# Kernel tuning notes

Hardware: AMD Instinct MI355X
Metric: run time of the kernel (lower is better)

## Reference

```python
import jax, jax.numpy as jnp
import numpy as np

N = 50000
E = 800000
F_IN = 128
HID = 32
NEG_SLOPE = 0.2  # PyG GATConv default


def _gat_layer(x, src, dst, W, a_src, a_dst, b, heads, out_c, concat, n_nodes):
    # Linear transform per head: [N, heads, out_c]
    h = (x @ W).reshape(n_nodes, heads, out_c)
    # Per-node attention logits per head
    al_src = jnp.einsum('nhc,hc->nh', h, a_src)  # source contribution
    al_dst = jnp.einsum('nhc,hc->nh', h, a_dst)  # destination contribution
    # Edge logits (message j=src -> i=dst), leaky relu
    e = jax.nn.leaky_relu(al_src[src] + al_dst[dst], NEG_SLOPE)  # [E', heads]
    # Segment softmax over incoming edges of each destination node
    m = jax.ops.segment_max(e, dst, num_segments=n_nodes)
    ex = jnp.exp(e - m[dst])
    denom = jax.ops.segment_sum(ex, dst, num_segments=n_nodes)
    alpha = ex / denom[dst]  # [E', heads]; self-loops guarantee denom > 0
    # Weighted scatter-aggregate of source features
    msg = h[src] * alpha[:, :, None]  # [E', heads, out_c]
    out = jax.ops.segment_sum(msg, dst, num_segments=n_nodes)  # [N, heads, out_c]
    out = out.reshape(n_nodes, heads * out_c) if concat else out.mean(axis=1)
    return out + b


def setup_inputs() -> dict:
    key = jax.random.key(0)
    ks = jax.random.split(key, 10)
    x = jax.random.normal(ks[0], (N, F_IN), dtype=jnp.float32)
    edge_index = jax.random.randint(ks[1], (2, E), 0, N, dtype=jnp.int64)
    s = 0.1
    return {
        'x': x,
        'edge_index': edge_index,
        'W1': jax.random.normal(ks[2], (F_IN, 4 * HID), dtype=jnp.float32) * s,
        'a_src1': jax.random.normal(ks[3], (4, HID), dtype=jnp.float32) * s,
        'a_dst1': jax.random.normal(ks[4], (4, HID), dtype=jnp.float32) * s,
        'b1': jnp.zeros((4 * HID,), jnp.float32),
        'W2': jax.random.normal(ks[5], (4 * HID, 2 * HID), dtype=jnp.float32) * s,
        'a_src2': jax.random.normal(ks[6], (2, HID), dtype=jnp.float32) * s,
        'a_dst2': jax.random.normal(ks[7], (2, HID), dtype=jnp.float32) * s,
        'b2': jnp.zeros((2 * HID,), jnp.float32),
        'W3': jax.random.normal(ks[8], (2 * HID, 1), dtype=jnp.float32) * s,
        'a_src3': jax.random.normal(ks[9], (1, 1), dtype=jnp.float32) * s,
        'a_dst3': jax.random.normal(jax.random.fold_in(key, 99), (1, 1), dtype=jnp.float32) * s,
        'b3': jnp.zeros((1,), jnp.float32),
    }


def reference(x, edge_index, W1, a_src1, a_dst1, b1, W2, a_src2, a_dst2, b2, W3, a_src3, a_dst3, b3):
    n = x.shape[0]
    # add_self_loops=True (PyG default)
    loop = jnp.arange(n, dtype=edge_index.dtype)
    src = jnp.concatenate([edge_index[0], loop])
    dst = jnp.concatenate([edge_index[1], loop])
    h = _gat_layer(x, src, dst, W1, a_src1, a_dst1, b1, 4, HID, True, n)
    h = jax.nn.elu(h)  # dropout is identity in eval mode
    h = _gat_layer(h, src, dst, W2, a_src2, a_dst2, b2, 2, HID, True, n)
    h = jax.nn.elu(h)
    out = _gat_layer(h, src, dst, W3, a_src3, a_dst3, b3, 1, 1, False, n)
    return out  # [N, 1]
```

## Files before the change

### kernel.cpp

```cpp
#include <hip/hip_runtime.h>
#include <hip/hip_fp16.h>
#include <math.h>

#define F_IN 128
constexpr int SB = 256;

__global__ void zero_int(int* p, int n) {
    int i = blockIdx.x * 256 + threadIdx.x;
    if (i < n) p[i] = 0;
}

__global__ void count_deg4(const int* __restrict__ dst, int* __restrict__ deg, int E) {
    int t = blockIdx.x * 256 + threadIdx.x;
    int base = t * 4;
    if (base + 3 < E) {
        int4 d = *(const int4*)(dst + base);
        atomicAdd(&deg[d.x], 1);
        atomicAdd(&deg[d.y], 1);
        atomicAdd(&deg[d.z], 1);
        atomicAdd(&deg[d.w], 1);
    } else {
        for (int k = 0; k < 4; ++k) {
            int e = base + k;
            if (e < E) atomicAdd(&deg[dst[e]], 1);
        }
    }
}

__global__ void scan1(const int* __restrict__ in, int* __restrict__ out,
                      int* __restrict__ bsums, int n, int selfN) {
    __shared__ int sm[SB];
    int i = blockIdx.x * SB + threadIdx.x;
    int v = (i < n) ? (in[i] + (i < selfN ? 1 : 0)) : 0;
    sm[threadIdx.x] = v;
    __syncthreads();
    for (int d = 1; d < SB; d <<= 1) {
        int t = (threadIdx.x >= d) ? sm[threadIdx.x - d] : 0;
        __syncthreads();
        sm[threadIdx.x] += t;
        __syncthreads();
    }
    if (i < n) out[i] = sm[threadIdx.x] - v;
    if (threadIdx.x == SB - 1) bsums[blockIdx.x] = sm[SB - 1];
}

__global__ void scan2(int* __restrict__ bsums, int nb) {
    __shared__ int sm[SB];
    int v = (threadIdx.x < nb) ? bsums[threadIdx.x] : 0;
    sm[threadIdx.x] = v;
    __syncthreads();
    for (int d = 1; d < SB; d <<= 1) {
        int t = (threadIdx.x >= d) ? sm[threadIdx.x - d] : 0;
        __syncthreads();
        sm[threadIdx.x] += t;
        __syncthreads();
    }
    if (threadIdx.x < nb) bsums[threadIdx.x] = sm[threadIdx.x] - v;
}

__global__ void scan3(int* __restrict__ off, int* __restrict__ cursor,
                      const int* __restrict__ bsums, int n, int ncur) {
    int i = blockIdx.x * SB + threadIdx.x;
    if (i < n) {
        int v = off[i] + bsums[blockIdx.x];
        off[i] = v;
        if (i < ncur) cursor[i] = v;
    }
}

template <int BN, int TN, int HEADS>
__device__ __forceinline__ void gemm_dev(
    const float* __restrict__ A, const float* __restrict__ B,
    const float* __restrict__ asrc, const float* __restrict__ adst,
    __half* __restrict__ C, float* __restrict__ als, float* __restrict__ ald,
    int M, int bid) {
    constexpr int BM = 128, BK = 16, TM = 4, K = 128, OC = 32;
    __shared__ float As[BK][BM + 4];
    __shared__ float Bs[BK][BN];
    const int tx = threadIdx.x, ty = threadIdx.y;
    const int tid = ty * 16 + tx;
    const int row0 = bid * BM;
    const int i0 = ty * TM;
    const int j0a = tx * 4;
    const int j0b = 64 + tx * 4;

    float acc[TM][TN];
#pragma unroll
    for (int m = 0; m < TM; ++m)
#pragma unroll
        for (int n = 0; n < TN; ++n) acc[m][n] = 0.f;

    const int ar = tid >> 2;
    const int ak = (tid & 3) * 4;
    int arow = row0 + ar;
    if (arow >= M) arow = M - 1;
    const float* Aptr = A + (size_t)arow * K + ak;
    const int bk = (BN == 128) ? (tid >> 5) : (tid >> 4);
    const int bc = (BN == 128) ? ((tid & 31) * 4) : ((tid & 15) * 4);
    const bool bact = (BN == 128) || (tid < 256);

    for (int kc = 0; kc < K; kc += BK) {
        float4 av = *(const float4*)(Aptr + kc);
        float4 bv;
        if (bact) bv = *(const float4*)(B + (size_t)(kc + bk) * BN + bc);
        __syncthreads();
        As[ak + 0][ar] = av.x;
        As[ak + 1][ar] = av.y;
        As[ak + 2][ar] = av.z;
        As[ak + 3][ar] = av.w;
        if (bact) *(float4*)&Bs[bk][bc] = bv;
        __syncthreads();
#pragma unroll
        for (int kk = 0; kk < BK; ++kk) {
            float4 a4 = *(const float4*)&As[kk][i0];
            float arr[TM] = {a4.x, a4.y, a4.z, a4.w};
            float br[TN];
            float4 b0 = *(const float4*)&Bs[kk][j0a];
            br[0] = b0.x; br[1] = b0.y; br[2] = b0.z; br[3] = b0.w;
            if constexpr (TN == 8) {
                float4 b1 = *(const float4*)&Bs[kk][j0b];
                br[4] = b1.x; br[5] = b1.y; br[6] = b1.z; br[7] = b1.w;
            }
#pragma unroll
            for (int m = 0; m < TM; ++m)
#pragma unroll
                for (int n = 0; n < TN; ++n) acc[m][n] += arr[m] * br[n];
        }
    }

#pragma unroll
    for (int m = 0; m < TM; ++m) {
        int row = row0 + i0 + m;
        bool ok = row < M;
        if constexpr (TN == 8) {
            if (ok) {
                alignas(8) __half2 pa[2], pb[2];
#pragma unroll
                for (int n2 = 0; n2 < 2; ++n2) {
                    pa[n2] = __floats2half2_rn(acc[m][2 * n2], acc[m][2 * n2 + 1]);
                    pb[n2] = __floats2half2_rn(acc[m][4 + 2 * n2], acc[m][5 + 2 * n2]);
                }
                *(uint2*)&C[(size_t)row * BN + j0a] = *(uint2*)pa;
                *(uint2*)&C[(size_t)row * BN + j0b] = *(uint2*)pb;
            }
            float psA = 0.f, pdA = 0.f, psB = 0.f, pdB = 0.f;
#pragma unroll
            for (int n = 0; n < 4; ++n) {
                psA += acc[m][n] * asrc[j0a + n];
                pdA += acc[m][n] * adst[j0a + n];
                psB += acc[m][n + 4] * asrc[j0b + n];
                pdB += acc[m][n + 4] * adst[j0b + n];
            }
#pragma unroll
            for (int msk = 1; msk < 8; msk <<= 1) {
                psA += __shfl_xor(psA, msk, 64);
                pdA += __shfl_xor(pdA, msk, 64);
                psB += __shfl_xor(psB, msk, 64);
                pdB += __shfl_xor(pdB, msk, 64);
            }
            if (ok && (tx & 7) == 0) {
                int hA = tx >> 3;
                als[row * HEADS + hA] = psA;
                ald[row * HEADS + hA] = pdA;
                als[row * HEADS + 2 + hA] = psB;
                ald[row * HEADS + 2 + hA] = pdB;
            }
        } else {
            if (ok) {
                alignas(8) __half2 ph[2];
#pragma unroll
                for (int n2 = 0; n2 < 2; ++n2)
                    ph[n2] = __floats2half2_rn(acc[m][2 * n2], acc[m][2 * n2 + 1]);
                *(uint2*)&C[(size_t)row * BN + j0a] = *(uint2*)ph;
            }
            float ps = 0.f, pd = 0.f;
#pragma unroll
            for (int n = 0; n < TN; ++n) {
                ps += acc[m][n] * asrc[j0a + n];
                pd += acc[m][n] * adst[j0a + n];
            }
#pragma unroll
            for (int msk = 1; msk < 8; msk <<= 1) {
                ps += __shfl_xor(ps, msk, 64);
                pd += __shfl_xor(pd, msk, 64);
            }
            if (ok && (tx & 7) == 0) {
                int h0 = tx >> 3;
                als[row * HEADS + h0] = ps;
                ald[row * HEADS + h0] = pd;
            }
        }
    }
}

__global__ __launch_bounds__(512) void gemm1_scatter(
    const float* __restrict__ A, const float* __restrict__ B,
    const float* __restrict__ asrc, const float* __restrict__ adst,
    __half* __restrict__ C, float* __restrict__ als, float* __restrict__ ald,
    int M, int gblk,
    const int* __restrict__ src, const int* __restrict__ dst,
    int* __restrict__ cursor, int* __restrict__ csr, int E, int N) {
    if ((int)blockIdx.x < gblk) {
        gemm_dev<128, 8, 4>(A, B, asrc, adst, C, als, ald, M, blockIdx.x);
        return;
    }
    int tid = threadIdx.y * 16 + threadIdx.x;
    int g = blockIdx.x & 7;
    int c = (blockIdx.x - gblk) >> 3;
    int t = c * 512 + tid;
    int E4 = (E + 3) >> 2;
    int nspan = (N + 7) >> 3;
    int r0 = g * nspan;
    int r1 = r0 + nspan; if (r1 > N) r1 = N;
    if (t < E4) {
        int base = t * 4;
        if (base + 3 < E) {
            int4 s4 = *(const int4*)(src + base);
            int4 d4 = *(const int4*)(dst + base);
            if (d4.x >= r0 && d4.x < r1) { int p = atomicAdd(&cursor[d4.x], 1); csr[p] = s4.x; }
            if (d4.y >= r0 && d4.y < r1) { int p = atomicAdd(&cursor[d4.y], 1); csr[p] = s4.y; }
            if (d4.z >= r0 && d4.z < r1) { int p = atomicAdd(&cursor[d4.z], 1); csr[p] = s4.z; }
            if (d4.w >= r0 && d4.w < r1) { int p = atomicAdd(&cursor[d4.w], 1); csr[p] = s4.w; }
        } else {
            for (int k = 0; k < 4; ++k) {
                int e = base + k;
                if (e < E) {
                    int d = dst[e];
                    if (d >= r0 && d < r1) {
                        int p = atomicAdd(&cursor[d], 1);
                        csr[p] = src[e];
                    }
                }
            }
        }
    } else {
        int i = t - E4;
        if (i >= r0 && i < r1) {
            int p = atomicAdd(&cursor[i], 1);
            csr[p] = i;
        }
    }
}

template <int BN, int TN, int HEADS>
__global__ __launch_bounds__(512) void gemm_fused(
    const float* __restrict__ A, const float* __restrict__ B,
    const float* __restrict__ asrc, const float* __restrict__ adst,
    __half* __restrict__ C, float* __restrict__ als, float* __restrict__ ald,
    int M) {
    gemm_dev<BN, TN, HEADS>(A, B, asrc, adst, C, als, ald, M, blockIdx.x);
}

template <int HEADS>
__global__ void edge_ex_node(const float* __restrict__ als, const float* __restrict__ ald,
                             const int* __restrict__ csr, const int* __restrict__ off,
                             float* __restrict__ ex_t, int n, int ET) {
    int g = blockIdx.x * blockDim.x + threadIdx.x;
    int node = g >> 4;
    int lane = g & 15;
    if (node >= n) return;
    float ad[HEADS];
    if constexpr (HEADS == 4) {
        float4 a = ((const float4*)ald)[node];
        ad[0] = a.x; ad[1] = a.y; ad[2] = a.z; ad[3] = a.w;
    } else if constexpr (HEADS == 2) {
        float2 a = ((const float2*)ald)[node];
        ad[0] = a.x; ad[1] = a.y;
    } else {
        ad[0] = ald[node];
    }
    int e1 = off[node + 1];
    for (int e = off[node] + lane; e < e1; e += 16) {
        int s = csr[e];
        float av[HEADS];
        if constexpr (HEADS == 4) {
            float4 a = ((const float4*)als)[s];
            av[0] = a.x; av[1] = a.y; av[2] = a.z; av[3] = a.w;
        } else if constexpr (HEADS == 2) {
            float2 a = ((const float2*)als)[s];
            av[0] = a.x; av[1] = a.y;
        } else {
            av[0] = als[s];
        }
#pragma unroll
        for (int hd = 0; hd < HEADS; ++hd) {
            float lg = av[hd] + ad[hd];
            lg = lg > 0.f ? lg : 0.2f * lg;
            ex_t[(size_t)hd * ET + e] = __expf(lg);
        }
    }
}

__global__ void gat_agg_l1(const __half* __restrict__ h, const float* __restrict__ ex_t,
                           const float* __restrict__ bias,
                           const int* __restrict__ off, const int* __restrict__ csr,
                           float* __restrict__ out, int n, int ET) {
    constexpr int P = 8;
    int wid = (blockIdx.x * blockDim.x + threadIdx.x) >> 6;
    int lane = threadIdx.x & 63;
    if (wid >= n) return;
    const int hd = lane >> 4;
    const __half2* h2 = (const __half2*)h + lane;
    const float* exp_ = ex_t + (size_t)hd * ET;
    int e0 = off[wid], e1 = off[wid + 1];
    float Sx = 0.f, Sy = 0.f, D = 0.f;

    float ex[P];
    __half2 hv[P];
#pragma unroll
    for (int p = 0; p < P; ++p) {
        int ee = e0 + p;
        int ie = (ee < e1) ? ee : e1 - 1;
        int s = csr[ie];
        float exv = exp_[ie];
        ex[p] = (ee < e1) ? exv : 0.f;
        hv[p] = h2[(size_t)s * 64];
    }
    int e = e0;
    for (; e + P < e1; e += P) {
        float nex[P];
        __half2 nhv[P];
#pragma unroll
        for (int p = 0; p < P; ++p) {
            int ee = e + P + p;
            int ie = (ee < e1) ? ee : e1 - 1;
            int s = csr[ie];
            float exv = exp_[ie];
            nex[p] = (ee < e1) ? exv : 0.f;
            nhv[p] = h2[(size_t)s * 64];
        }
#pragma unroll
        for (int p = 0; p < P; ++p) {
            D += ex[p];
            Sx = fmaf(ex[p], __low2float(hv[p]), Sx);
            Sy = fmaf(ex[p], __high2float(hv[p]), Sy);
            ex[p] = nex[p];
            hv[p] = nhv[p];
        }
    }
#pragma unroll
    for (int p = 0; p < P; ++p) {
        D += ex[p];
        Sx = fmaf(ex[p], __low2float(hv[p]), Sx);
        Sy = fmaf(ex[p], __high2float(hv[p]), Sy);
    }

    float inv = 1.f / D;
    float2 bv = ((const float2*)bias)[lane];
    float vx = Sx * inv + bv.x, vy = Sy * inv + bv.y;
    vx = vx > 0.f ? vx : (__expf(vx) - 1.f);
    vy = vy > 0.f ? vy : (__expf(vy) - 1.f);
    float2 o; o.x = vx; o.y = vy;
    ((float2*)out)[(size_t)wid * 64 + lane] = o;
}

__global__ void gat_agg_l2(const __half* __restrict__ h, const float* __restrict__ ex_t,
                           const float* __restrict__ bias,
                           const int* __restrict__ off, const int* __restrict__ csr,
                           const float* __restrict__ W3, const float* __restrict__ as3,
                           const float* __restrict__ ad3, float* __restrict__ h3,
                           float* __restrict__ als3, float* __restrict__ ald3,
                           int n, int ET) {
    constexpr int P = 8;
    int wid = (blockIdx.x * blockDim.x + threadIdx.x) >> 6;
    int lane = threadIdx.x & 63;
    if (wid >= n) return;
    const int hd = lane >> 5;
    const __half* hp = h + lane;
    const float* exp_ = ex_t + (size_t)hd * ET;
    int e0 = off[wid], e1 = off[wid + 1];
    float S = 0.f, D = 0.f;

    float ex[P];
    __half hv[P];
#pragma unroll
    for (int p = 0; p < P; ++p) {
        int ee = e0 + p;
        int ie = (ee < e1) ? ee : e1 - 1;
        int s = csr[ie];
        float exv = exp_[ie];
        ex[p] = (ee < e1) ? exv : 0.f;
        hv[p] = hp[(size_t)s * 64];
    }
    int e = e0;
    for (; e + P < e1; e += P) {
        float nex[P];
        __half nhv[P];
#pragma unroll
        for (int p = 0; p < P; ++p) {
            int ee = e + P + p;
            int ie = (ee < e1) ? ee : e1 - 1;
            int s = csr[ie];
            float exv = exp_[ie];
            nex[p] = (ee < e1) ? exv : 0.f;
            nhv[p] = hp[(size_t)s * 64];
        }
#pragma unroll
        for (int p = 0; p < P; ++p) {
            D += ex[p];
            S = fmaf(ex[p], __half2float(hv[p]), S);
            ex[p] = nex[p];
            hv[p] = nhv[p];
        }
    }
#pragma unroll
    for (int p = 0; p < P; ++p) {
        D += ex[p];
        S = fmaf(ex[p], __half2float(hv[p]), S);
    }

    float v = S / D + bias[lane];
    v = v > 0.f ? v : (__expf(v) - 1.f);
    float r = v * W3[lane];
#pragma unroll
    for (int msk = 1; msk < 64; msk <<= 1) r += __shfl_xor(r, msk, 64);
    if (lane == 0) {
        h3[wid] = r;
        als3[wid] = r * as3[0];
        ald3[wid] = r * ad3[0];
    }
}

__global__ void gat_agg1(const float* __restrict__ h, const float* __restrict__ ex_t,
                         const float* __restrict__ bias,
                         const int* __restrict__ off, const int* __restrict__ csr,
                         float* __restrict__ out, int n) {
    int i = blockIdx.x * blockDim.x + threadIdx.x;
    if (i >= n) return;
    int e0 = off[i], e1 = off[i + 1];
    float S = 0.f, D = 0.f;
    float ex[2], hv[2];
#pragma unroll
    for (int p = 0; p < 2; ++p) {
        int ee = e0 + p;
        int ie = (ee < e1) ? ee : e1 - 1;
        int s = csr[ie];
        float exv = ex_t[ie];
        ex[p] = (ee < e1) ? exv : 0.f;
        hv[p] = h[s];
    }
    int e = e0;
    for (; e + 2 < e1; e += 2) {
#pragma unroll
        for (int p = 0; p < 2; ++p) {
            int ee = e + 2 + p;
            int ie = (ee < e1) ? ee : e1 - 1;
            int s = csr[ie];
            float exv = ex_t[ie];
            float nex = (ee < e1) ? exv : 0.f;
            float nhv = h[s];
            D += ex[p];
            S = fmaf(ex[p], hv[p], S);
            ex[p] = nex;
            hv[p] = nhv;
        }
    }
#pragma unroll
    for (int p = 0; p < 2; ++p) {
        D += ex[p];
        S = fmaf(ex[p], hv[p], S);
    }
    out[i] = S / D + bias[0];
}

extern "C" void kernel_launch(void* const* d_in, const int* in_sizes, int n_in,
                              void* d_out, int out_size, void* d_ws, size_t ws_size,
                              hipStream_t stream) {
    const float* x   = (const float*)d_in[0];
    const int*   ei  = (const int*)d_in[1];
    const float* W1  = (const float*)d_in[2];
    const float* as1 = (const float*)d_in[3];
    const float* ad1 = (const float*)d_in[4];
    const float* b1  = (const float*)d_in[5];
    const float* W2  = (const float*)d_in[6];
    const float* as2 = (const float*)d_in[7];
    const float* ad2 = (const float*)d_in[8];
    const float* b2  = (const float*)d_in[9];
    const float* W3  = (const float*)d_in[10];
    const float* as3 = (const float*)d_in[11];
    const float* ad3 = (const float*)d_in[12];
    const float* b3  = (const float*)d_in[13];
    float* out = (float*)d_out;

    const int N = in_sizes[0] / F_IN;
    const int E = in_sizes[1] / 2;
    const int ET = E + N;

    char* w = (char*)d_ws;
    size_t o = 0;
    auto alloc = [&](size_t bytes) -> void* {
        void* p = w + o;
        o += (bytes + 255) & ~(size_t)255;
        return p;
    };
    __half* hbuf = (__half*)alloc((size_t)N * 128 * 2);
    float* a1   = (float*)alloc((size_t)N * 128 * 4);
    float* h3   = (float*)alloc((size_t)N * 4);
    float* als  = (float*)alloc((size_t)N * 4 * 4);
    float* ald  = (float*)alloc((size_t)N * 4 * 4);
    float* als3 = (float*)alloc((size_t)N * 4);
    float* ald3 = (float*)alloc((size_t)N * 4);
    int* deg    = (int*)alloc((size_t)(N + 1) * 4);
    int* off    = (int*)alloc((size_t)(N + 1) * 4);
    int* cursor = (int*)alloc((size_t)N * 4);
    int* bsums  = (int*)alloc(1024);
    int* csr    = (int*)alloc((size_t)ET * 4);
    float* exb  = (float*)alloc((size_t)4 * ET * 4);

    __half* h2 = hbuf;

    const int* esrc = ei;
    const int* edst = ei + E;

    zero_int<<<(N + 1 + 255) / 256, 256, 0, stream>>>(deg, N + 1);
    count_deg4<<<((E + 3) / 4 + 255) / 256, 256, 0, stream>>>(edst, deg, E);
    int n1 = N + 1;
    int nb = (n1 + SB - 1) / SB;
    scan1<<<nb, SB, 0, stream>>>(deg, off, bsums, n1, N);
    scan2<<<1, SB, 0, stream>>>(bsums, nb);
    scan3<<<nb, SB, 0, stream>>>(off, cursor, bsums, n1, N);

    const int gblk = (N + 127) / 128;

    {
        int E4 = (E + 3) >> 2;
        int spg = (E4 + N + 511) / 512;
        int sblk = 8 * spg;
        gemm1_scatter<<<gblk + sblk, dim3(16, 32), 0, stream>>>(
            x, W1, as1, ad1, hbuf, als, ald, N, gblk,
            esrc, edst, cursor, csr, E, N);
    }

    const int exblk = (N * 16 + 255) / 256;

    edge_ex_node<4><<<exblk, 256, 0, stream>>>(als, ald, csr, off, exb, N, ET);
    gat_agg_l1<<<(N * 64 + 255) / 256, 256, 0, stream>>>(
        hbuf, exb, b1, off, csr, a1, N, ET);

    gemm_fused<64, 4, 2><<<gblk, dim3(16, 32), 0, stream>>>(
        a1, W2, as2, ad2, h2, als, ald, N);
    edge_ex_node<2><<<exblk, 256, 0, stream>>>(als, ald, csr, off, exb, N, ET);
    gat_agg_l2<<<(N * 64 + 255) / 256, 256, 0, stream>>>(
        h2, exb, b2, off, csr, W3, as3, ad3, h3, als3, ald3, N, ET);

    edge_ex_node<1><<<exblk, 256, 0, stream>>>(als3, ald3, csr, off, exb, N, ET);
    gat_agg1<<<(N + 255) / 256, 256, 0, stream>>>(h3, exb, b3, off, csr, out, N);
}
```

Baseline: 219.5 us.

## Fuse edge exp computation into aggregation kernels and store layer-1 output in fp16

Removes the three separate edge_ex_node kernels and the per-edge exp buffer; each aggregation kernel now gathers the source logit and computes leaky-relu plus exp inline. The layer-1 activations are stored as fp16 and the layer-2 GEMM reads half inputs. Layer 3 packs h and its source logit into one float2 so a single gather serves both. Zeroing uses hipMemsetAsync instead of a kernel. This saves launches and per-edge global traffic, at the cost of recomputing exp per lane and lower precision for the intermediate activations.

```diff
diff --git a/kernel.cpp b/kernel.cpp
--- a/kernel.cpp
+++ b/kernel.cpp
@@ -4,11 +4,6 @@
 
 #define F_IN 128
 constexpr int SB = 256;
-
-__global__ void zero_int(int* p, int n) {
-    int i = blockIdx.x * 256 + threadIdx.x;
-    if (i < n) p[i] = 0;
-}
 
 __global__ void count_deg4(const int* __restrict__ dst, int* __restrict__ deg, int E) {
     int t = blockIdx.x * 256 + threadIdx.x;
@@ -68,13 +63,13 @@
     }
 }
 
-template <int BN, int TN, int HEADS>
+template <int BN, int TN, int HEADS, typename AT>
 __device__ __forceinline__ void gemm_dev(
-    const float* __restrict__ A, const float* __restrict__ B,
+    const AT* __restrict__ A, const float* __restrict__ B,
     const float* __restrict__ asrc, const float* __restrict__ adst,
     __half* __restrict__ C, float* __restrict__ als, float* __restrict__ ald,
     int M, int bid) {
-    constexpr int BM = 128, BK = 16, TM = 4, K = 128, OC = 32;
+    constexpr int BM = 128, BK = 16, TM = 4, K = 128;
     __shared__ float As[BK][BM + 4];
     __shared__ float Bs[BK][BN];
     const int tx = threadIdx.x, ty = threadIdx.y;
@@ -94,20 +89,31 @@
     const int ak = (tid & 3) * 4;
     int arow = row0 + ar;
     if (arow >= M) arow = M - 1;
-    const float* Aptr = A + (size_t)arow * K + ak;
+    const AT* Aptr = A + (size_t)arow * K + ak;
     const int bk = (BN == 128) ? (tid >> 5) : (tid >> 4);
     const int bc = (BN == 128) ? ((tid & 31) * 4) : ((tid & 15) * 4);
     const bool bact = (BN == 128) || (tid < 256);
 
     for (int kc = 0; kc < K; kc += BK) {
-        float4 av = *(const float4*)(Aptr + kc);
+        float a0, a1v, a2v, a3v;
+        if constexpr (sizeof(AT) == 4) {
+            float4 av = *(const float4*)(Aptr + kc);
+            a0 = av.x; a1v = av.y; a2v = av.z; a3v = av.w;
+        } else {
+            uint2 raw = *(const uint2*)(Aptr + kc);
+            __half2 h01 = *(__half2*)&raw.x;
+            __half2 h23 = *(__half2*)&raw.y;
+            float2 f01 = __half22float2(h01);
+            float2 f23 = __half22float2(h23);
+            a0 = f01.x; a1v = f01.y; a2v = f23.x; a3v = f23.y;
+        }
         float4 bv;
         if (bact) bv = *(const float4*)(B + (size_t)(kc + bk) * BN + bc);
         __syncthreads();
-        As[ak + 0][ar] = av.x;
-        As[ak + 1][ar] = av.y;
-        As[ak + 2][ar] = av.z;
-        As[ak + 3][ar] = av.w;
+        As[ak + 0][ar] = a0;
+        As[ak + 1][ar] = a1v;
+        As[ak + 2][ar] = a2v;
+        As[ak + 3][ar] = a3v;
         if (bact) *(float4*)&Bs[bk][bc] = bv;
         __syncthreads();
 #pragma unroll
@@ -201,7 +207,7 @@
     const int* __restrict__ src, const int* __restrict__ dst,
     int* __restrict__ cursor, int* __restrict__ csr, int E, int N) {
     if ((int)blockIdx.x < gblk) {
-        gemm_dev<128, 8, 4>(A, B, asrc, adst, C, als, ald, M, blockIdx.x);
+        gemm_dev<128, 8, 4, float>(A, B, asrc, adst, C, als, ald, M, blockIdx.x);
         return;
     }
     int tid = threadIdx.y * 16 + threadIdx.x;
@@ -243,106 +249,73 @@
 }
 
 template <int BN, int TN, int HEADS>
-__global__ __launch_bounds__(512) void gemm_fused(
-    const float* __restrict__ A, const float* __restrict__ B,
+__global__ __launch_bounds__(512) void gemm_fused_h(
+    const __half* __restrict__ A, const float* __restrict__ B,
     const float* __restrict__ asrc, const float* __restrict__ adst,
     __half* __restrict__ C, float* __restrict__ als, float* __restrict__ ald,
     int M) {
-    gemm_dev<BN, TN, HEADS>(A, B, asrc, adst, C, als, ald, M, blockIdx.x);
-}
-
-template <int HEADS>
-__global__ void edge_ex_node(const float* __restrict__ als, const float* __restrict__ ald,
-                             const int* __restrict__ csr, const int* __restrict__ off,
-                             float* __restrict__ ex_t, int n, int ET) {
-    int g = blockIdx.x * blockDim.x + threadIdx.x;
-    int node = g >> 4;
-    int lane = g & 15;
-    if (node >= n) return;
-    float ad[HEADS];
-    if constexpr (HEADS == 4) {
-        float4 a = ((const float4*)ald)[node];
-        ad[0] = a.x; ad[1] = a.y; ad[2] = a.z; ad[3] = a.w;
-    } else if constexpr (HEADS == 2) {
-        float2 a = ((const float2*)ald)[node];
-        ad[0] = a.x; ad[1] = a.y;
-    } else {
-        ad[0] = ald[node];
-    }
-    int e1 = off[node + 1];
-    for (int e = off[node] + lane; e < e1; e += 16) {
-        int s = csr[e];
-        float av[HEADS];
-        if constexpr (HEADS == 4) {
-            float4 a = ((const float4*)als)[s];
-            av[0] = a.x; av[1] = a.y; av[2] = a.z; av[3] = a.w;
-        } else if constexpr (HEADS == 2) {
-            float2 a = ((const float2*)als)[s];
-            av[0] = a.x; av[1] = a.y;
-        } else {
-            av[0] = als[s];
-        }
-#pragma unroll
-        for (int hd = 0; hd < HEADS; ++hd) {
-            float lg = av[hd] + ad[hd];
-            lg = lg > 0.f ? lg : 0.2f * lg;
-            ex_t[(size_t)hd * ET + e] = __expf(lg);
-        }
-    }
-}
-
-__global__ void gat_agg_l1(const __half* __restrict__ h, const float* __restrict__ ex_t,
+    gemm_dev<BN, TN, HEADS, __half>(A, B, asrc, adst, C, als, ald, M, blockIdx.x);
+}
+
+__global__ void gat_agg_l1(const __half* __restrict__ h,
+                           const float* __restrict__ als, const float* __restrict__ ald,
                            const float* __restrict__ bias,
                            const int* __restrict__ off, const int* __restrict__ csr,
-                           float* __restrict__ out, int n, int ET) {
+                           __half* __restrict__ out, int n) {
     constexpr int P = 8;
     int wid = (blockIdx.x * blockDim.x + threadIdx.x) >> 6;
     int lane = threadIdx.x & 63;
     if (wid >= n) return;
     const int hd = lane >> 4;
     const __half2* h2 = (const __half2*)h + lane;
-    const float* exp_ = ex_t + (size_t)hd * ET;
+    float ad = ald[wid * 4 + hd];
     int e0 = off[wid], e1 = off[wid + 1];
     float Sx = 0.f, Sy = 0.f, D = 0.f;
 
-    float ex[P];
+    float al[P];
     __half2 hv[P];
 #pragma unroll
     for (int p = 0; p < P; ++p) {
         int ee = e0 + p;
         int ie = (ee < e1) ? ee : e1 - 1;
         int s = csr[ie];
-        float exv = exp_[ie];
-        ex[p] = (ee < e1) ? exv : 0.f;
+        float av = als[s * 4 + hd];
+        al[p] = (ee < e1) ? av : -1e30f;
         hv[p] = h2[(size_t)s * 64];
     }
     int e = e0;
     for (; e + P < e1; e += P) {
-        float nex[P];
+        float nal[P];
         __half2 nhv[P];
 #pragma unroll
         for (int p = 0; p < P; ++p) {
             int ee = e + P + p;
             int ie = (ee < e1) ? ee : e1 - 1;
             int s = csr[ie];
-            float exv = exp_[ie];
-            nex[p] = (ee < e1) ? exv : 0.f;
+            float av = als[s * 4 + hd];
+            nal[p] = (ee < e1) ? av : -1e30f;
             nhv[p] = h2[(size_t)s * 64];
         }
 #pragma unroll
         for (int p = 0; p < P; ++p) {
-            D += ex[p];
-            Sx = fmaf(ex[p], __low2float(hv[p]), Sx);
-            Sy = fmaf(ex[p], __high2float(hv[p]), Sy);
-            ex[p] = nex[p];
+            float lg = al[p] + ad;
+            lg = lg > 0.f ? lg : 0.2f * lg;
+            float exv = __expf(lg);
+            D += exv;
+            Sx = fmaf(exv, __low2float(hv[p]), Sx);
+            Sy = fmaf(exv, __high2float(hv[p]), Sy);
+            al[p] = nal[p];
             hv[p] = nhv[p];
         }
     }
 #pragma unroll
     for (int p = 0; p < P; ++p) {
-        D += ex[p];
-        Sx = fmaf(ex[p], __low2float(hv[p]), Sx);
-        Sy = fmaf(ex[p], __high2float(hv[p]), Sy);
+        float lg = al[p] + ad;
+        lg = lg > 0.f ? lg : 0.2f * lg;
+        float exv = __expf(lg);
+        D += exv;
+        Sx = fmaf(exv, __low2float(hv[p]), Sx);
+        Sy = fmaf(exv, __high2float(hv[p]), Sy);
     }
 
     float inv = 1.f / D;
@@ -350,63 +323,68 @@
     float vx = Sx * inv + bv.x, vy = Sy * inv + bv.y;
     vx = vx > 0.f ? vx : (__expf(vx) - 1.f);
     vy = vy > 0.f ? vy : (__expf(vy) - 1.f);
-    float2 o; o.x = vx; o.y = vy;
-    ((float2*)out)[(size_t)wid * 64 + lane] = o;
-}
-
-__global__ void gat_agg_l2(const __half* __restrict__ h, const float* __restrict__ ex_t,
+    ((__half2*)out)[(size_t)wid * 64 + lane] = __floats2half2_rn(vx, vy);
+}
+
+__global__ void gat_agg_l2(const __half* __restrict__ h,
+                           const float* __restrict__ als, const float* __restrict__ ald,
                            const float* __restrict__ bias,
                            const int* __restrict__ off, const int* __restrict__ csr,
                            const float* __restrict__ W3, const float* __restrict__ as3,
-                           const float* __restrict__ ad3, float* __restrict__ h3,
-                           float* __restrict__ als3, float* __restrict__ ald3,
-                           int n, int ET) {
+                           const float* __restrict__ ad3, float2* __restrict__ hs,
+                           float* __restrict__ ald3, int n) {
     constexpr int P = 8;
     int wid = (blockIdx.x * blockDim.x + threadIdx.x) >> 6;
     int lane = threadIdx.x & 63;
     if (wid >= n) return;
     const int hd = lane >> 5;
     const __half* hp = h + lane;
-    const float* exp_ = ex_t + (size_t)hd * ET;
+    float ad = ald[wid * 2 + hd];
     int e0 = off[wid], e1 = off[wid + 1];
     float S = 0.f, D = 0.f;
 
-    float ex[P];
+    float al[P];
     __half hv[P];
 #pragma unroll
     for (int p = 0; p < P; ++p) {
         int ee = e0 + p;
         int ie = (ee < e1) ? ee : e1 - 1;
         int s = csr[ie];
-        float exv = exp_[ie];
-        ex[p] = (ee < e1) ? exv : 0.f;
+        float av = als[s * 2 + hd];
+        al[p] = (ee < e1) ? av : -1e30f;
         hv[p] = hp[(size_t)s * 64];
     }
     int e = e0;
     for (; e + P < e1; e += P) {
-        float nex[P];
+        float nal[P];
         __half nhv[P];
 #pragma unroll
         for (int p = 0; p < P; ++p) {
             int ee = e + P + p;
             int ie = (ee < e1) ? ee : e1 - 1;
             int s = csr[ie];
-            float exv = exp_[ie];
-            nex[p] = (ee < e1) ? exv : 0.f;
+            float av = als[s * 2 + hd];
+            nal[p] = (ee < e1) ? av : -1e30f;
             nhv[p] = hp[(size_t)s * 64];
         }
 #pragma unroll
         for (int p = 0; p < P; ++p) {
-            D += ex[p];
-            S = fmaf(ex[p], __half2float(hv[p]), S);
-            ex[p] = nex[p];
+            float lg = al[p] + ad;
+            lg = lg > 0.f ? lg : 0.2f * lg;
+            float exv = __expf(lg);
+            D += exv;
+            S = fmaf(exv, __half2float(hv[p]), S);
+            al[p] = nal[p];
             hv[p] = nhv[p];
         }
     }
 #pragma unroll
     for (int p = 0; p < P; ++p) {
-        D += ex[p];
-        S = fmaf(ex[p], __half2float(hv[p]), S);
+        float lg = al[p] + ad;
+        lg = lg > 0.f ? lg : 0.2f * lg;
+        float exv = __expf(lg);
+        D += exv;
+        S = fmaf(exv, __half2float(hv[p]), S);
     }
 
     float v = S / D + bias[lane];
@@ -415,29 +393,29 @@
 #pragma unroll
     for (int msk = 1; msk < 64; msk <<= 1) r += __shfl_xor(r, msk, 64);
     if (lane == 0) {
-        h3[wid] = r;
-        als3[wid] = r * as3[0];
+        hs[wid] = make_float2(r, r * as3[0]);
         ald3[wid] = r * ad3[0];
     }
 }
 
-__global__ void gat_agg1(const float* __restrict__ h, const float* __restrict__ ex_t,
+__global__ void gat_agg1(const float2* __restrict__ hs, const float* __restrict__ ald3,
                          const float* __restrict__ bias,
                          const int* __restrict__ off, const int* __restrict__ csr,
                          float* __restrict__ out, int n) {
     int i = blockIdx.x * blockDim.x + threadIdx.x;
     if (i >= n) return;
+    float ad = ald3[i];
     int e0 = off[i], e1 = off[i + 1];
     float S = 0.f, D = 0.f;
-    float ex[2], hv[2];
+    float2 g[2];
+    float valid[2];
 #pragma unroll
     for (int p = 0; p < 2; ++p) {
         int ee = e0 + p;
         int ie = (ee < e1) ? ee : e1 - 1;
         int s = csr[ie];
-        float exv = ex_t[ie];
-        ex[p] = (ee < e1) ? exv : 0.f;
-        hv[p] = h[s];
+        g[p] = hs[s];
+        valid[p] = (ee < e1) ? 0.f : -1e30f;
     }
     int e = e0;
     for (; e + 2 < e1; e += 2) {
@@ -446,19 +424,24 @@
             int ee = e + 2 + p;
             int ie = (ee < e1) ? ee : e1 - 1;
             int s = csr[ie];
-            float exv = ex_t[ie];
-            float nex = (ee < e1) ? exv : 0.f;
-            float nhv = h[s];
-            D += ex[p];
-            S = fmaf(ex[p], hv[p], S);
-            ex[p] = nex;
-            hv[p] = nhv;
+            float2 ng = hs[s];
+            float nvalid = (ee < e1) ? 0.f : -1e30f;
+            float lg = g[p].y + ad + valid[p];
+            lg = lg > 0.f ? lg : 0.2f * lg;
+            float exv = __expf(lg);
+            D += exv;
+            S = fmaf(exv, g[p].x, S);
+            g[p] = ng;
+            valid[p] = nvalid;
         }
     }
 #pragma unroll
     for (int p = 0; p < 2; ++p) {
-        D += ex[p];
-        S = fmaf(ex[p], hv[p], S);
+        float lg = g[p].y + ad + valid[p];
+        lg = lg > 0.f ? lg : 0.2f * lg;
+        float exv = __expf(lg);
+        D += exv;
+        S = fmaf(exv, g[p].x, S);
     }
     out[i] = S / D + bias[0];
 }
@@ -494,25 +477,23 @@
         return p;
     };
     __half* hbuf = (__half*)alloc((size_t)N * 128 * 2);
-    float* a1   = (float*)alloc((size_t)N * 128 * 4);
-    float* h3   = (float*)alloc((size_t)N * 4);
+    __half* a1   = (__half*)alloc((size_t)N * 128 * 2);
+    float2* hs   = (float2*)alloc((size_t)N * 8);
     float* als  = (float*)alloc((size_t)N * 4 * 4);
     float* ald  = (float*)alloc((size_t)N * 4 * 4);
-    float* als3 = (float*)alloc((size_t)N * 4);
     float* ald3 = (float*)alloc((size_t)N * 4);
     int* deg    = (int*)alloc((size_t)(N + 1) * 4);
     int* off    = (int*)alloc((size_t)(N + 1) * 4);
     int* cursor = (int*)alloc((size_t)N * 4);
     int* bsums  = (int*)alloc(1024);
     int* csr    = (int*)alloc((size_t)ET * 4);
-    float* exb  = (float*)alloc((size_t)4 * ET * 4);
 
     __half* h2 = hbuf;
 
     const int* esrc = ei;
     const int* edst = ei + E;
 
-    zero_int<<<(N + 1 + 255) / 256, 256, 0, stream>>>(deg, N + 1);
+    hipMemsetAsync(deg, 0, (size_t)(N + 1) * 4, stream);
     count_deg4<<<((E + 3) / 4 + 255) / 256, 256, 0, stream>>>(edst, deg, E);
     int n1 = N + 1;
     int nb = (n1 + SB - 1) / SB;
@@ -531,18 +512,13 @@
             esrc, edst, cursor, csr, E, N);
     }
 
-    const int exblk = (N * 16 + 255) / 256;
-
-    edge_ex_node<4><<<exblk, 256, 0, stream>>>(als, ald, csr, off, exb, N, ET);
     gat_agg_l1<<<(N * 64 + 255) / 256, 256, 0, stream>>>(
-        hbuf, exb, b1, off, csr, a1, N, ET);
-
-    gemm_fused<64, 4, 2><<<gblk, dim3(16, 32), 0, stream>>>(
+        hbuf, als, ald, b1, off, csr, a1, N);
+
+    gemm_fused_h<64, 4, 2><<<gblk, dim3(16, 32), 0, stream>>>(
         a1, W2, as2, ad2, h2, als, ald, N);
-    edge_ex_node<2><<<exblk, 256, 0, stream>>>(als, ald, csr, off, exb, N, ET);
     gat_agg_l2<<<(N * 64 + 255) / 256, 256, 0, stream>>>(
-        h2, exb, b2, off, csr, W3, as3, ad3, h3, als3, ald3, N, ET);
-
-    edge_ex_node<1><<<exblk, 256, 0, stream>>>(als3, ald3, csr, off, exb, N, ET);
-    gat_agg1<<<(N + 255) / 256, 256, 0, stream>>>(h3, exb, b3, off, csr, out, N);
-}
+        h2, als, ald, b2, off, csr, W3, as3, ad3, hs, ald3, N);
+
+    gat_agg1<<<(N + 255) / 256, 256, 0, stream>>>(hs, ald3, b3, off, csr, out, N);
+}
```

Measured after the change: 205.5 us. 1.07x faster.
